# Performance work log

Hardware: AMD Instinct MI355X
Metric: run time of the kernel (lower is better)

The kernel has to match this reference:

```python
import jax, jax.numpy as jnp
import numpy as np

STRIDE = 1
PADDING = 1
GROUPS = 1


def setup_inputs() -> dict:
    key = jax.random.key(0)
    kx, kw, kb = jax.random.split(key, 3)
    x_int = jax.random.randint(kx, (16, 256, 56, 56), 0, 127, dtype=jnp.int32)
    weight_int = jax.random.randint(kw, (256, 256, 3, 3), 0, 127, dtype=jnp.int32)
    bias_int = jax.random.randint(kb, (256,), 0, 127, dtype=jnp.int32)
    return {"x_int": x_int, "weight_int": weight_int, "bias_int": bias_int}


def reference(x_int, weight_int, bias_int):
    # Integer conv2d with int32 accumulation, exactly F.conv2d semantics.
    y = jax.lax.conv_general_dilated(
        x_int,
        weight_int,
        window_strides=(STRIDE, STRIDE),
        padding=((PADDING, PADDING), (PADDING, PADDING)),
        dimension_numbers=("NCHW", "OIHW", "NCHW"),
        feature_group_count=GROUPS,
    )
    # bias broadcast over [B, Cout, H, W]
    return y + bias_int[None, :, None, None]
```

## Files before the change

### kernel.cpp

```cpp
#include <hip/hip_runtime.h>


typedef int v4i  __attribute__((ext_vector_type(4)));
typedef int v16i __attribute__((ext_vector_type(16)));

#define X8_ROWSTRIDE 1856
#define X8_IMGSTRIDE 107648
#define X8_BYTES     13778944
#define W8_CHUNK     18432
#define WBUF         18432
#define XBUF         20480
#define LBUF         38912

typedef const __attribute__((address_space(1))) unsigned char* gptr_t;
typedef __attribute__((address_space(3))) unsigned char* lptr_t;

__device__ __forceinline__ void gll(const unsigned char* g, unsigned char* l) {
  __builtin_amdgcn_global_load_lds((gptr_t)g, (lptr_t)l, 16, 0, 0);
}

__device__ __forceinline__ int pack4(const int* p, int stride) {
  return (p[0] & 255) | ((p[stride] & 255) << 8) |
         ((p[2 * stride] & 255) << 16) | ((p[3 * stride] & 255) << 24);
}

__global__ __launch_bounds__(256)
void pack_all(const int* __restrict__ x, const int* __restrict__ wgt,
              unsigned char* __restrict__ ws8) {
  const int blk = blockIdx.x;
  if (blk < 784) {
    const int gid = blk * 256 + threadIdx.x;
    const int srcg = gid & 1;
    int t = gid >> 1;
    const int sq = t % 14;  t /= 14;
    const int row = t % 56 + 1;
    const int cb  = t / 56;
    const int chunk = cb >> 4, b = cb & 15;
    const int ci0 = chunk * 32 + srcg * 16;
    const int* src = x + (b * 256 + ci0) * 3136 + (row - 1) * 56 + 4 * sq;
    v4i L[16];
    #pragma unroll
    for (int ch = 0; ch < 16; ++ch) L[ch] = *(const v4i*)(src + ch * 3136);
    unsigned char* dstrow = ws8 + cb * X8_IMGSTRIDE + row * X8_ROWSTRIDE;
    #pragma unroll
    for (int j = 0; j < 4; ++j) {
      const int slot = 4 * sq + 1 + j;
      v4i g;
      #pragma unroll
      for (int d = 0; d < 4; ++d)
        g[d] = (L[4 * d][j] & 255) | ((L[4 * d + 1][j] & 255) << 8) |
               ((L[4 * d + 2][j] & 255) << 16) | ((L[4 * d + 3][j] & 255) << 24);
      const int p = (srcg + (slot >> 2)) & 1;
      *(v4i*)(dstrow + slot * 32 + p * 16) = g;
    }
  } else if (blk < 1012) {
    const int g2 = (blk - 784) * 256 + threadIdx.x;
    const int cb = g2 / 456;
    const int r  = g2 - cb * 456;
    int off;
    if (r < 232) {
      const int row = r < 116 ? 0 : 57;
      const int rr = r % 116;
      off = row * X8_ROWSTRIDE + (rr >> 1) * 32 + (rr & 1) * 16;
    } else {
      const int r2 = r - 232;
      const int row = (r2 >> 2) + 1;
      const int slot = (r2 & 2) ? 57 : 0;
      off = row * X8_ROWSTRIDE + slot * 32 + (r2 & 1) * 16;
    }
    *(v4i*)(ws8 + cb * X8_IMGSTRIDE + off) = (v4i){0, 0, 0, 0};
  } else {
    const int gw = (blk - 1012) * 256 + threadIdx.x;
    const int p = gw & 1;
    int t = gw >> 1;
    const int tap = t % 9;  t /= 9;
    const int co = t & 63;
    const int tcc = t >> 6;
    const int chunk = tcc & 7, cotile = tcc >> 3;
    const int srcg = (p + (co >> 2)) & 1;
    const int ci0 = chunk * 32 + srcg * 16;
    const int* src = wgt + ((cotile * 64 + co) * 256 + ci0) * 9 + tap;
    v4i v = (v4i){pack4(src, 9), pack4(src + 36, 9),
                  pack4(src + 72, 9), pack4(src + 108, 9)};
    *(v4i*)(ws8 + X8_BYTES + (t * 9 + tap) * 32 + p * 16) = v;
  }
}

__device__ __forceinline__ void stage_chunk(const unsigned char* wg,
                                            const unsigned char* xg,
                                            unsigned char* ldsb, int c, int buf,
                                            int tid) {
  const unsigned char* wsrc = wg + c * W8_CHUNK;
  const unsigned char* xsrc = xg + c * (16 * X8_IMGSTRIDE);
  unsigned char* wdst = ldsb + buf * LBUF;
  unsigned char* xdst = wdst + WBUF;
  #pragma unroll
  for (int i = 0; i < 4; ++i) {
    const int o = (tid + i * 256) * 16;
    gll(wsrc + o, wdst + o);
  }
  if (tid < 128) {
    const int o = (1024 + tid) * 16;
    gll(wsrc + o, wdst + o);
  } else {
    const int o = (tid - 128) * 16;
    gll(xsrc + o, xdst + o);
  }
  #pragma unroll
  for (int i = 5; i < 9; ++i) {
    const int o = (tid + i * 256 - 1152) * 16;
    gll(xsrc + o, xdst + o);
  }
  if (tid < 128) {
    const int o = (1152 + tid) * 16;
    gll(xsrc + o, xdst + o);
  }
}

#define LOADTAP(T, S)                                                     \
  do {                                                                    \
    const int kh_ = (T) / 3, kw_ = (T) % 3;                               \
    const unsigned char* xr_ = xs + rbase + kh_ * X8_ROWSTRIDE;           \
    fa0[S] = *(const v4i*)(wls + abase + (T) * 32);                       \
    fa1[S] = *(const v4i*)(wls + 9216 + abase + (T) * 32);                \
    fb[S][0] = *(const v4i*)(xr_ + boff[kw_][0]);                         \
    fb[S][1] = *(const v4i*)(xr_ + boff[kw_][1]);                         \
    fb[S][2] = *(const v4i*)(xr_ + boff[kw_][2]);                         \
    fb[S][3] = *(const v4i*)(xr_ + boff[kw_][3]);                         \
  } while (0)

__global__ __launch_bounds__(256, 2)
void conv_main(const unsigned char* __restrict__ ws8, const int* __restrict__ bias,
               int* __restrict__ out) {
  __shared__ __align__(16) unsigned char lds[2 * LBUF];
  __shared__ int bls[64];

  const int tid = threadIdx.x, lane = tid & 63, wv = tid >> 6;
  const int n = lane & 31, gq = lane >> 5;
  const int tc = blockIdx.y;
  const int hb = blockIdx.x;
  const int hg = hb >> 4, b = hb & 15;
  const int h0 = hg * 8;

  if (tid < 64) {
    bls[tid] = bias[tc * 64 + tid];
    asm volatile("s_waitcnt lgkmcnt(0)" ::: "memory");
  }

  const int abase = n * 288 + (((gq + (n >> 2)) & 1) << 4);
  int boff[3][4];
  #pragma unroll
  for (int kw = 0; kw < 3; ++kw)
    #pragma unroll
    for (int bt = 0; bt < 4; ++bt) {
      int slot = bt * 16 + (n & 15) + kw;
      if (slot > 57) slot = 57;
      boff[kw][bt] = slot * 32 + (((gq + (slot >> 2)) & 1) << 4);
    }
  const int rbase = (2 * wv + (n >> 4)) * X8_ROWSTRIDE;

  v16i acc[2][4];
  #pragma unroll
  for (int i = 0; i < 2; ++i)
    #pragma unroll
    for (int j = 0; j < 4; ++j)
      acc[i][j] = (v16i){0,0,0,0,0,0,0,0,0,0,0,0,0,0,0,0};

  const unsigned char* wg = ws8 + X8_BYTES + tc * (8 * W8_CHUNK);
  const unsigned char* xg = ws8 + b * X8_IMGSTRIDE + h0 * X8_ROWSTRIDE;

  stage_chunk(wg, xg, lds, 0, 0, tid);
  int buf = 0;
  #pragma unroll 1
  for (int c = 0; c < 8; ++c) {
    asm volatile("s_waitcnt vmcnt(0)" ::: "memory");
    __builtin_amdgcn_s_barrier();
    asm volatile("" ::: "memory");
    if (c < 7) stage_chunk(wg, xg, lds, c + 1, buf ^ 1, tid);
    {
      const unsigned char* wls = lds + buf * LBUF;
      const unsigned char* xs  = wls + WBUF;
      v4i fa0[2], fa1[2], fb[2][4];
      LOADTAP(0, 0);
      __builtin_amdgcn_sched_group_barrier(0x100, 6, 0);
      #pragma unroll
      for (int tap = 0; tap < 9; ++tap) {
        const int cur = tap & 1, nxt = cur ^ 1;
        if (tap < 8) LOADTAP(tap + 1, nxt);
        if (tap < 8)
          __builtin_amdgcn_sched_group_barrier(0x100, 6, 0);
        #pragma unroll
        for (int bt = 0; bt < 4; ++bt) {
          acc[0][bt] = __builtin_amdgcn_mfma_i32_32x32x32_i8(fa0[cur], fb[cur][bt], acc[0][bt], 0, 0, 0);
          acc[1][bt] = __builtin_amdgcn_mfma_i32_32x32x32_i8(fa1[cur], fb[cur][bt], acc[1][bt], 0, 0, 0);
        }
        __builtin_amdgcn_sched_group_barrier(0x008, 8, 0);
      }
    }
    buf ^= 1;
  }

  const int h = h0 + 2 * wv + (n >> 4);
  const int wbase = lane & 15;
  #pragma unroll
  for (int ct = 0; ct < 2; ++ct) {
    #pragma unroll
    for (int r = 0; r < 16; ++r) {
      const int co64 = ct * 32 + (r & 3) + 8 * (r >> 2) + 4 * gq;
      const int bv = bls[co64];
      int* orow = out + ((b * 256 + tc * 64 + co64) * 56 + h) * 56;
      #pragma unroll
      for (int bt = 0; bt < 4; ++bt) {
        const int w0 = bt * 16 + wbase;
        if (w0 < 56) orow[w0] = acc[ct][bt][r] + bv;
      }
    }
  }
}

extern "C" void kernel_launch(void* const* d_in, const int* in_sizes, int n_in,
                              void* d_out, int out_size, void* d_ws, size_t ws_size,
                              hipStream_t stream) {
  const int* x    = (const int*)d_in[0];
  const int* w    = (const int*)d_in[1];
  const int* bias = (const int*)d_in[2];
  unsigned char* ws8 = (unsigned char*)d_ws;
  hipLaunchKernelGGL(pack_all, dim3(1156), dim3(256), 0, stream, x, w, ws8);
  hipLaunchKernelGGL(conv_main, dim3(112, 4, 1), dim3(256), 0, stream,
                     ws8, bias, (int*)d_out);
}
```

Before: 130.2 us.

## Load weight fragments directly from global into registers, bypassing LDS

Weights are repacked into an MFMA-fragment-friendly layout (tap-major, per-lane contiguous 32-byte slots) so each lane can read its A operand for all 9 taps straight from global/L2 into registers at the start of each chunk. LDS now only holds the input tile, cutting the LDS footprint per stage and removing the weight LDS reads. The cost is 18 extra VGPR-quad registers per thread and global-load latency exposed at each chunk start, since the loads sit after the barrier and are not prefetched.

```diff
diff --git a/kernel.cpp b/kernel.cpp
--- a/kernel.cpp
+++ b/kernel.cpp
@@ -8,9 +8,7 @@
 #define X8_IMGSTRIDE 107648
 #define X8_BYTES     13778944
 #define W8_CHUNK     18432
-#define WBUF         18432
 #define XBUF         20480
-#define LBUF         38912
 
 typedef const __attribute__((address_space(1))) unsigned char* gptr_t;
 typedef __attribute__((address_space(3))) unsigned char* lptr_t;
@@ -73,56 +71,35 @@
     const int gw = (blk - 1012) * 256 + threadIdx.x;
     const int p = gw & 1;
     int t = gw >> 1;
-    const int tap = t % 9;  t /= 9;
     const int co = t & 63;
-    const int tcc = t >> 6;
-    const int chunk = tcc & 7, cotile = tcc >> 3;
-    const int srcg = (p + (co >> 2)) & 1;
-    const int ci0 = chunk * 32 + srcg * 16;
+    int u = t >> 6;
+    const int tap = u % 9;
+    const int cc = u / 9;
+    const int chunk = cc & 7, cotile = cc >> 3;
+    const int ci0 = chunk * 32 + p * 16;
     const int* src = wgt + ((cotile * 64 + co) * 256 + ci0) * 9 + tap;
     v4i v = (v4i){pack4(src, 9), pack4(src + 36, 9),
                   pack4(src + 72, 9), pack4(src + 108, 9)};
-    *(v4i*)(ws8 + X8_BYTES + (t * 9 + tap) * 32 + p * 16) = v;
-  }
-}
-
-__device__ __forceinline__ void stage_chunk(const unsigned char* wg,
-                                            const unsigned char* xg,
+    *(v4i*)(ws8 + X8_BYTES + t * 32 + p * 16) = v;
+  }
+}
+
+__device__ __forceinline__ void stage_chunk(const unsigned char* xg,
                                             unsigned char* ldsb, int c, int buf,
                                             int tid) {
-  const unsigned char* wsrc = wg + c * W8_CHUNK;
   const unsigned char* xsrc = xg + c * (16 * X8_IMGSTRIDE);
-  unsigned char* wdst = ldsb + buf * LBUF;
-  unsigned char* xdst = wdst + WBUF;
-  #pragma unroll
-  for (int i = 0; i < 4; ++i) {
+  unsigned char* xdst = ldsb + buf * XBUF;
+  #pragma unroll
+  for (int i = 0; i < 5; ++i) {
     const int o = (tid + i * 256) * 16;
-    gll(wsrc + o, wdst + o);
-  }
-  if (tid < 128) {
-    const int o = (1024 + tid) * 16;
-    gll(wsrc + o, wdst + o);
-  } else {
-    const int o = (tid - 128) * 16;
     gll(xsrc + o, xdst + o);
   }
-  #pragma unroll
-  for (int i = 5; i < 9; ++i) {
-    const int o = (tid + i * 256 - 1152) * 16;
-    gll(xsrc + o, xdst + o);
-  }
-  if (tid < 128) {
-    const int o = (1152 + tid) * 16;
-    gll(xsrc + o, xdst + o);
-  }
-}
-
-#define LOADTAP(T, S)                                                     \
+}
+
+#define LOADB(T, S)                                                       \
   do {                                                                    \
-    const int kh_ = (T) / 3, kw_ = (T) % 3;                               \
-    const unsigned char* xr_ = xs + rbase + kh_ * X8_ROWSTRIDE;           \
-    fa0[S] = *(const v4i*)(wls + abase + (T) * 32);                       \
-    fa1[S] = *(const v4i*)(wls + 9216 + abase + (T) * 32);                \
+    const int kw_ = (T) % 3;                                              \
+    const unsigned char* xr_ = xs + rbase + ((T) / 3) * X8_ROWSTRIDE;     \
     fb[S][0] = *(const v4i*)(xr_ + boff[kw_][0]);                         \
     fb[S][1] = *(const v4i*)(xr_ + boff[kw_][1]);                         \
     fb[S][2] = *(const v4i*)(xr_ + boff[kw_][2]);                         \
@@ -132,7 +109,7 @@
 __global__ __launch_bounds__(256, 2)
 void conv_main(const unsigned char* __restrict__ ws8, const int* __restrict__ bias,
                int* __restrict__ out) {
-  __shared__ __align__(16) unsigned char lds[2 * LBUF];
+  __shared__ __align__(16) unsigned char lds[2 * XBUF];
   __shared__ int bls[64];
 
   const int tid = threadIdx.x, lane = tid & 63, wv = tid >> 6;
@@ -147,7 +124,7 @@
     asm volatile("s_waitcnt lgkmcnt(0)" ::: "memory");
   }
 
-  const int abase = n * 288 + (((gq + (n >> 2)) & 1) << 4);
+  const int aoff = n * 32 + gq * 16;
   int boff[3][4];
   #pragma unroll
   for (int kw = 0; kw < 3; ++kw)
@@ -169,30 +146,37 @@
   const unsigned char* wg = ws8 + X8_BYTES + tc * (8 * W8_CHUNK);
   const unsigned char* xg = ws8 + b * X8_IMGSTRIDE + h0 * X8_ROWSTRIDE;
 
-  stage_chunk(wg, xg, lds, 0, 0, tid);
+  stage_chunk(xg, lds, 0, 0, tid);
   int buf = 0;
   #pragma unroll 1
   for (int c = 0; c < 8; ++c) {
     asm volatile("s_waitcnt vmcnt(0)" ::: "memory");
     __builtin_amdgcn_s_barrier();
     asm volatile("" ::: "memory");
-    if (c < 7) stage_chunk(wg, xg, lds, c + 1, buf ^ 1, tid);
+    const unsigned char* wgc = wg + c * W8_CHUNK;
+    v4i A0[9], A1[9];
+    #pragma unroll
+    for (int t = 0; t < 9; ++t) {
+      A0[t] = *(const v4i*)(wgc + t * 2048 + aoff);
+      A1[t] = *(const v4i*)(wgc + t * 2048 + 1024 + aoff);
+    }
+    if (c < 7) stage_chunk(xg, lds, c + 1, buf ^ 1, tid);
     {
-      const unsigned char* wls = lds + buf * LBUF;
-      const unsigned char* xs  = wls + WBUF;
-      v4i fa0[2], fa1[2], fb[2][4];
-      LOADTAP(0, 0);
-      __builtin_amdgcn_sched_group_barrier(0x100, 6, 0);
+      const unsigned char* xs = lds + buf * XBUF;
+      v4i fb[2][4];
+      LOADB(0, 0);
+      __builtin_amdgcn_sched_group_barrier(0x100, 4, 0);
       #pragma unroll
       for (int tap = 0; tap < 9; ++tap) {
         const int cur = tap & 1, nxt = cur ^ 1;
-        if (tap < 8) LOADTAP(tap + 1, nxt);
-        if (tap < 8)
-          __builtin_amdgcn_sched_group_barrier(0x100, 6, 0);
+        if (tap < 8) {
+          LOADB(tap + 1, nxt);
+          __builtin_amdgcn_sched_group_barrier(0x100, 4, 0);
+        }
         #pragma unroll
         for (int bt = 0; bt < 4; ++bt) {
-          acc[0][bt] = __builtin_amdgcn_mfma_i32_32x32x32_i8(fa0[cur], fb[cur][bt], acc[0][bt], 0, 0, 0);
-          acc[1][bt] = __builtin_amdgcn_mfma_i32_32x32x32_i8(fa1[cur], fb[cur][bt], acc[1][bt], 0, 0, 0);
+          acc[0][bt] = __builtin_amdgcn_mfma_i32_32x32x32_i8(A0[tap], fb[cur][bt], acc[0][bt], 0, 0, 0);
+          acc[1][bt] = __builtin_amdgcn_mfma_i32_32x32x32_i8(A1[tap], fb[cur][bt], acc[1][bt], 0, 0, 0);
         }
         __builtin_amdgcn_sched_group_barrier(0x008, 8, 0);
       }
```

After: 139.4 us. 1.07x slower.
